# Kernel optimization log

Hardware: AMD Instinct MI355X
Metric: run time of the kernel (lower is better)

Reference implementation:

```python
import jax, jax.numpy as jnp
import numpy as np

HIDDEN = 2048
N_HEADS = 16
HEAD_DIM = HIDDEN // N_HEADS  # 128
ROTARY_DIM = 32
ROPE_BASE = 10000.0
NEG_INF = -10000.0  # matches torch code's additive mask constant


def setup_inputs() -> dict:
    key = jax.random.key(0)
    k1, k2, k3 = jax.random.split(key, 3)
    x = jax.random.normal(k1, (2, 2048, HIDDEN), dtype=jnp.float32)
    # scale weights like nn.Linear default init (uniform ~ 1/sqrt(fan_in))
    Wqkv_w = jax.random.normal(k2, (3 * HIDDEN, HIDDEN), dtype=jnp.float32) * (1.0 / np.sqrt(HIDDEN))
    Wqkv_b = jax.random.normal(k3, (3 * HIDDEN,), dtype=jnp.float32) * 0.01
    return {"x": x, "Wqkv_w": Wqkv_w, "Wqkv_b": Wqkv_b}


def _rope_cos_sin(seqlen, dtype):
    inv_freq = 1.0 / (ROPE_BASE ** (jnp.arange(0, ROTARY_DIM, 2, dtype=jnp.float32) / ROTARY_DIM))
    t = jnp.arange(seqlen, dtype=jnp.float32)
    freqs = jnp.outer(t, inv_freq)  # (S, ROTARY_DIM//2)
    return jnp.cos(freqs).astype(dtype), jnp.sin(freqs).astype(dtype)


def _apply_rotary(u, cos, sin):
    # u: (B, S, H, D); rotate first ROTARY_DIM dims, GPT-NeoX half-split style
    u_rot, u_pass = u[..., :ROTARY_DIM], u[..., ROTARY_DIM:]
    u1, u2 = u_rot[..., : ROTARY_DIM // 2], u_rot[..., ROTARY_DIM // 2 :]
    c = cos[None, :, None, :]  # (1, S, 1, ROTARY_DIM//2)
    s = sin[None, :, None, :]
    rot = jnp.concatenate([u1 * c - u2 * s, u1 * s + u2 * c], axis=-1)
    return jnp.concatenate([rot, u_pass], axis=-1)


def reference(x, Wqkv_w, Wqkv_b):
    B, S, _ = x.shape
    qkv = jnp.einsum("bse,oe->bso", x, Wqkv_w) + Wqkv_b  # (B, S, 3*H*D)
    qkv = qkv.reshape(B, S, 3, N_HEADS, HEAD_DIM)
    cos, sin = _rope_cos_sin(S, x.dtype)
    q = _apply_rotary(qkv[:, :, 0], cos, sin)
    k = _apply_rotary(qkv[:, :, 1], cos, sin)
    v = qkv[:, :, 2]
    scale = 1.0 / np.sqrt(HEAD_DIM)
    scores = jnp.einsum("bthd,bshd->bhts", q, k * scale)  # (B, H, T, S)
    causal_mask = jnp.triu(jnp.full((S, S), NEG_INF, dtype=scores.dtype), 1)
    scores = scores + causal_mask
    attn = jax.nn.softmax(scores, axis=-1)
    out = jnp.einsum("bhts,bshd->bthd", attn, v)  # (B, S, H, D)
    return out.reshape(B, S, N_HEADS * HEAD_DIM)
```

## Files before the change

### kernel.cpp

```cpp
#include <hip/hip_runtime.h>

#define B_    2
#define S_    2048
#define E_    2048
#define NH_   16
#define HD_   128
#define NQKV_ 6144
#define M_    4096
#define XN_   (M_ * E_)

typedef short bf16x8 __attribute__((ext_vector_type(8)));
typedef float f32x4  __attribute__((ext_vector_type(4)));

typedef const __attribute__((address_space(1))) void* gas_t;
typedef __attribute__((address_space(3))) void*       las_t;

__device__ inline float b2f(unsigned short u) {
    return __uint_as_float(((unsigned int)u) << 16);
}
__device__ inline unsigned short f2b(float f) {
    unsigned int x = __float_as_uint(f);
    x = x + 0x7fffu + ((x >> 16) & 1u);
    return (unsigned short)(x >> 16);
}
__device__ inline unsigned int pk2(float lo, float hi) {
    return (unsigned int)f2b(lo) | ((unsigned int)f2b(hi) << 16);
}

__global__ __launch_bounds__(256) void cvt_bf16(
    const float* __restrict__ X,
    const float* __restrict__ W,
    unsigned short* __restrict__ O)
{
    const long i = (long)(blockIdx.x * 256 + threadIdx.x) * 8;
    const float* src = (i < XN_) ? (X + i) : (W + (i - XN_));
    const float4 a = *(const float4*)(src);
    const float4 b = *(const float4*)(src + 4);
    uint4 o = { pk2(a.x, a.y), pk2(a.z, a.w), pk2(b.x, b.y), pk2(b.z, b.w) };
    *(uint4*)(O + i) = o;
}

__global__ __launch_bounds__(256, 2) void qkv_gemm(
    const unsigned short* __restrict__ Xb,
    const unsigned short* __restrict__ Wb,
    const float* __restrict__ bias,
    unsigned short* __restrict__ qb,
    unsigned short* __restrict__ kb,
    unsigned short* __restrict__ vb)
{
    __shared__ __align__(16) unsigned short As[2][128 * 32];
    __shared__ __align__(16) unsigned short Bs[2][128 * 32];

    const int t    = threadIdx.x;
    const int lane = t & 63;
    const int w    = t >> 6;
    const int m0   = blockIdx.y * 128;
    const int n0   = blockIdx.x * 128;
    const int wm   = (w >> 1) * 64;
    const int wn   = (w & 1) * 64;
    const int quad = lane >> 4;
    const int l16  = lane & 15;

    const unsigned short* Ag = Xb + (size_t)(m0 + (lane >> 2)) * E_ + (lane & 3) * 8;
    const unsigned short* Bg = Wb + (size_t)(n0 + (lane >> 2)) * E_ + (lane & 3) * 8;

    auto stage = [&](int bsel, int k0) {
        #pragma unroll
        for (int u = 0; u < 2; u++) {
            const int r0 = (w * 2 + u) * 16;
            __builtin_amdgcn_global_load_lds(
                (gas_t)(Ag + (size_t)r0 * E_ + k0),
                (las_t)&As[bsel][r0 * 32], 16, 0, 0);
            __builtin_amdgcn_global_load_lds(
                (gas_t)(Bg + (size_t)r0 * E_ + k0),
                (las_t)&Bs[bsel][r0 * 32], 16, 0, 0);
        }
    };

    f32x4 acc[4][4];
    #pragma unroll
    for (int i = 0; i < 4; i++)
        #pragma unroll
        for (int j = 0; j < 4; j++)
            #pragma unroll
            for (int r = 0; r < 4; r++) acc[i][j][r] = 0.0f;

    stage(0, 0);
    __syncthreads();
    int cur = 0;

    for (int k0 = 0; k0 < E_; k0 += 32) {
        if (k0 + 32 < E_) stage(cur ^ 1, k0 + 32);

        bf16x8 af[4], bfr[4];
        #pragma unroll
        for (int i = 0; i < 4; i++)
            af[i]  = *(const bf16x8*)&As[cur][(wm + i * 16 + l16) * 32 + quad * 8];
        #pragma unroll
        for (int i = 0; i < 4; i++)
            bfr[i] = *(const bf16x8*)&Bs[cur][(wn + i * 16 + l16) * 32 + quad * 8];

        #pragma unroll
        for (int i = 0; i < 4; i++)
            #pragma unroll
            for (int j = 0; j < 4; j++)
                acc[i][j] = __builtin_amdgcn_mfma_f32_16x16x32_bf16(
                    af[i], bfr[j], acc[i][j], 0, 0, 0);

        __syncthreads();
        cur ^= 1;
    }

    const int nb0   = n0 + wn;
    const int which = nb0 >> 11;
    const int h     = (nb0 >> 7) & 15;
    unsigned short* dst = (which == 0) ? qb : ((which == 1) ? kb : vb);

    float bv[4];
    #pragma unroll
    for (int j = 0; j < 4; j++) bv[j] = bias[nb0 + j * 16 + l16];
    #pragma unroll
    for (int i = 0; i < 4; i++)
        #pragma unroll
        for (int j = 0; j < 4; j++)
            #pragma unroll
            for (int r = 0; r < 4; r++) acc[i][j][r] += bv[j];

    if (wn == 0 && which < 2) {
        const float inv = exp2f(-0.83048202372184059f * (float)l16);
        #pragma unroll
        for (int i = 0; i < 4; i++) {
            #pragma unroll
            for (int r = 0; r < 4; r++) {
                const int m = m0 + wm + i * 16 + quad * 4 + r;
                const int s = m & (S_ - 1);
                float c, sn;
                __sincosf((float)s * inv, &sn, &c);
                const float u1 = acc[i][0][r], u2 = acc[i][1][r];
                acc[i][0][r] = u1 * c - u2 * sn;
                acc[i][1][r] = u1 * sn + u2 * c;
            }
        }
    }

    #pragma unroll
    for (int j = 0; j < 4; j++) {
        const int d = wn + j * 16 + l16;
        #pragma unroll
        for (int i = 0; i < 4; i++) {
            #pragma unroll
            for (int r = 0; r < 4; r++) {
                const int m  = m0 + wm + i * 16 + quad * 4 + r;
                const int bb = m >> 11;
                const int s  = m & (S_ - 1);
                dst[((size_t)(bb * NH_ + h) * S_ + s) * HD_ + d] = f2b(acc[i][j][r]);
            }
        }
    }
}

#define KSTR 136
#define VSTR 72
#define PSTR 72
#define OSTR 132

__global__ __launch_bounds__(256, 2) void attn_mfma(
    const unsigned short* __restrict__ qb,
    const unsigned short* __restrict__ kb,
    const unsigned short* __restrict__ vb,
    float* __restrict__ out)
{
    union SM {
        struct {
            unsigned short Ks[64 * KSTR];
            unsigned short Vt[128 * VSTR];
            unsigned short Ps[4 * 32 * PSTR];
        } a;
        float Ow[4 * 16 * OSTR];
    };
    __shared__ __align__(16) SM sm;
    unsigned short* Ks = sm.a.Ks;
    unsigned short* Vt = sm.a.Vt;
    unsigned short* Ps = sm.a.Ps;

    const int bid  = blockIdx.x;
    const int qt   = (S_ / 128 - 1) - (bid >> 5);
    const int bh   = bid & 31;
    const int b    = bh >> 4;
    const int h    = bh & 15;
    const int t    = threadIdx.x;
    const int lane = t & 63;
    const int w    = t >> 6;
    const int quad = lane >> 4;
    const int l16  = lane & 15;

    const int qb0    = qt * 128;
    const int wrow0  = qb0 + w * 32;
    const int ntiles = 2 * qt + 2;

    unsigned short* Pw = Ps + w * 32 * PSTR;

    const int krow = t >> 2, kcb = (t & 3) * 32;
    const int vq   = t & 31, vd0 = (t >> 5) * 16;

    bf16x8 qf[2][4];
    #pragma unroll
    for (int mb = 0; mb < 2; mb++) {
        const unsigned short* qp =
            qb + ((size_t)(bh * S_ + wrow0 + mb * 16 + l16)) * HD_ + quad * 8;
        #pragma unroll
        for (int c = 0; c < 4; c++)
            qf[mb][c] = *(const bf16x8*)(qp + c * 32);
    }

    f32x4 of[2][8];
    #pragma unroll
    for (int mb = 0; mb < 2; mb++)
        #pragma unroll
        for (int db = 0; db < 8; db++)
            #pragma unroll
            for (int r = 0; r < 4; r++) of[mb][db][r] = 0.0f;
    float mr[2][4], lr[2][4];
    #pragma unroll
    for (int mb = 0; mb < 2; mb++)
        #pragma unroll
        for (int r = 0; r < 4; r++) { mr[mb][r] = -1e30f; lr[mb][r] = 0.0f; }

    const float scale2 = 0.12751744459892879f;
    const float mneg2  = -14426.950408889634f;

    uint4 kr[4];
    uint4 v0a, v0b, v1a, v1b;

    auto issue_tile = [&](int kt2) {
        const int s2 = kt2 * 64;
        const unsigned short* kg = kb + ((size_t)(bh * S_ + s2 + krow)) * HD_ + kcb;
        #pragma unroll
        for (int u = 0; u < 4; u++) kr[u] = *(const uint4*)(kg + u * 8);
        const unsigned short* vg = vb + ((size_t)(bh * S_ + s2 + 2 * vq)) * HD_ + vd0;
        v0a = *(const uint4*)(vg);
        v0b = *(const uint4*)(vg + 8);
        v1a = *(const uint4*)(vg + HD_);
        v1b = *(const uint4*)(vg + HD_ + 8);
    };

    issue_tile(0);

    for (int kt = 0; kt < ntiles; kt++) {
        const int s0 = kt * 64;
        __syncthreads();
        #pragma unroll
        for (int u = 0; u < 4; u++)
            *(uint4*)&Ks[krow * KSTR + kcb + u * 8] = kr[u];
        {
            unsigned int r0[8] = { v0a.x, v0a.y, v0a.z, v0a.w,
                                   v0b.x, v0b.y, v0b.z, v0b.w };
            unsigned int r1[8] = { v1a.x, v1a.y, v1a.z, v1a.w,
                                   v1b.x, v1b.y, v1b.z, v1b.w };
            #pragma unroll
            for (int j = 0; j < 16; j++) {
                const int u = j >> 1;
                unsigned int pk;
                if ((j & 1) == 0)
                    pk = (r0[u] & 0xffffu) | (r1[u] << 16);
                else
                    pk = (r0[u] >> 16) | (r1[u] & 0xffff0000u);
                *(unsigned int*)&Vt[(vd0 + j) * VSTR + 2 * vq] = pk;
            }
        }
        __syncthreads();

        if (kt + 1 < ntiles) issue_tile(kt + 1);

        f32x4 sf[2][4];
        #pragma unroll
        for (int mb = 0; mb < 2; mb++)
            #pragma unroll
            for (int nb = 0; nb < 4; nb++)
                #pragma unroll
                for (int r = 0; r < 4; r++) sf[mb][nb][r] = 0.0f;
        #pragma unroll
        for (int c = 0; c < 4; c++) {
            #pragma unroll
            for (int nb = 0; nb < 4; nb++) {
                bf16x8 kf = *(const bf16x8*)&Ks[(nb * 16 + l16) * KSTR + c * 32 + quad * 8];
                #pragma unroll
                for (int mb = 0; mb < 2; mb++)
                    sf[mb][nb] = __builtin_amdgcn_mfma_f32_16x16x32_bf16(
                        qf[mb][c], kf, sf[mb][nb], 0, 0, 0);
            }
        }

        const bool need_mask = (s0 + 63 > wrow0);
        #pragma unroll
        for (int mb = 0; mb < 2; mb++) {
            const int qr0 = wrow0 + mb * 16 + quad * 4;
            #pragma unroll
            for (int nb = 0; nb < 4; nb++) {
                const int kcol = s0 + nb * 16 + l16;
                #pragma unroll
                for (int r = 0; r < 4; r++) {
                    float s = sf[mb][nb][r] * scale2;
                    if (need_mask && kcol > qr0 + r) s += mneg2;
                    sf[mb][nb][r] = s;
                }
            }
        }

        #pragma unroll
        for (int mb = 0; mb < 2; mb++) {
            float mt4[4];
            #pragma unroll
            for (int r = 0; r < 4; r++) {
                float mt = fmaxf(fmaxf(sf[mb][0][r], sf[mb][1][r]),
                                 fmaxf(sf[mb][2][r], sf[mb][3][r]));
                mt = fmaxf(mt, __shfl_xor(mt, 1));
                mt = fmaxf(mt, __shfl_xor(mt, 2));
                mt = fmaxf(mt, __shfl_xor(mt, 4));
                mt = fmaxf(mt, __shfl_xor(mt, 8));
                mt4[r] = mt;
            }
            const bool grew = (mt4[0] > mr[mb][0]) || (mt4[1] > mr[mb][1]) ||
                              (mt4[2] > mr[mb][2]) || (mt4[3] > mr[mb][3]);
            if (__any(grew)) {
                float alpha[4];
                #pragma unroll
                for (int r = 0; r < 4; r++) {
                    const float mnew = fmaxf(mr[mb][r], mt4[r]);
                    alpha[r] = __builtin_amdgcn_exp2f(mr[mb][r] - mnew);
                    mr[mb][r] = mnew;
                    lr[mb][r] *= alpha[r];
                }
                #pragma unroll
                for (int db = 0; db < 8; db++)
                    #pragma unroll
                    for (int r = 0; r < 4; r++) of[mb][db][r] *= alpha[r];
            }
            #pragma unroll
            for (int r = 0; r < 4; r++) {
                float rs = 0.0f;
                #pragma unroll
                for (int nb = 0; nb < 4; nb++) {
                    float p = __builtin_amdgcn_exp2f(sf[mb][nb][r] - mr[mb][r]);
                    sf[mb][nb][r] = p;
                    rs += p;
                }
                lr[mb][r] += rs;
            }

            #pragma unroll
            for (int nb = 0; nb < 4; nb++)
                #pragma unroll
                for (int r = 0; r < 4; r++)
                    Pw[(mb * 16 + quad * 4 + r) * PSTR + nb * 16 + l16] =
                        f2b(sf[mb][nb][r]);
        }

        #pragma unroll
        for (int kc = 0; kc < 2; kc++) {
            bf16x8 pf[2];
            #pragma unroll
            for (int mb = 0; mb < 2; mb++)
                pf[mb] = *(const bf16x8*)&Pw[(mb * 16 + l16) * PSTR + kc * 32 + quad * 8];
            #pragma unroll
            for (int db = 0; db < 8; db++) {
                bf16x8 vf = *(const bf16x8*)&Vt[(db * 16 + l16) * VSTR + kc * 32 + quad * 8];
                #pragma unroll
                for (int mb = 0; mb < 2; mb++)
                    of[mb][db] = __builtin_amdgcn_mfma_f32_16x16x32_bf16(
                        pf[mb], vf, of[mb][db], 0, 0, 0);
            }
        }
    }

    float* Ow = sm.Ow + w * 16 * OSTR;
    #pragma unroll
    for (int mb = 0; mb < 2; mb++) {
        __syncthreads();
        float inv[4];
        #pragma unroll
        for (int r = 0; r < 4; r++) {
            float ls = lr[mb][r];
            ls += __shfl_xor(ls, 1);
            ls += __shfl_xor(ls, 2);
            ls += __shfl_xor(ls, 4);
            ls += __shfl_xor(ls, 8);
            inv[r] = 1.0f / ls;
        }
        #pragma unroll
        for (int db = 0; db < 8; db++)
            #pragma unroll
            for (int r = 0; r < 4; r++)
                Ow[(quad * 4 + r) * OSTR + db * 16 + l16] = of[mb][db][r] * inv[r];
        #pragma unroll
        for (int rg = 0; rg < 4; rg++) {
            const int rowl = rg * 4 + quad;
            float* op = out + ((size_t)(b * S_ + wrow0 + mb * 16 + rowl)) * E_ + h * HD_;
            #pragma unroll
            for (int u = 0; u < 2; u++) {
                float4 v4 = *(const float4*)&Ow[rowl * OSTR + u * 64 + l16 * 4];
                *(float4*)(op + u * 64 + l16 * 4) = v4;
            }
        }
    }
}

extern "C" void kernel_launch(void* const* d_in, const int* in_sizes, int n_in,
                              void* d_out, int out_size, void* d_ws, size_t ws_size,
                              hipStream_t stream)
{
    const float* x    = (const float*)d_in[0];
    const float* W    = (const float*)d_in[1];
    const float* bias = (const float*)d_in[2];
    float* out = (float*)d_out;

    const size_t per = (size_t)B_ * NH_ * S_ * HD_;
    unsigned short* qb = (unsigned short*)d_ws;
    unsigned short* kb = qb + per;
    unsigned short* vb = kb + per;
    unsigned short* Xb = vb + per;
    unsigned short* Wb = Xb + (size_t)XN_;

    const int cvt_elems = XN_ + NQKV_ * E_;
    cvt_bf16<<<cvt_elems / (256 * 8), 256, 0, stream>>>(x, W, Xb);

    dim3 gemm_grid(NQKV_ / 128, M_ / 128);
    qkv_gemm<<<gemm_grid, 256, 0, stream>>>(Xb, Wb, bias, qb, kb, vb);

    attn_mfma<<<dim3((S_ / 128) * B_ * NH_), 256, 0, stream>>>(qb, kb, vb, out);
}
```

Measured before the change: 381.6 us.

## Shrink attention query tile to 64 rows per block, doubling grid size

Each attention block now handles 64 query rows (16 per wave) instead of 128 (32 per wave), and the grid grows to 1024 blocks. Per-thread accumulators and the P staging buffer are halved, and launch bounds now request 3 blocks per CU, aiming for better occupancy and load balance on the causal triangle. In exchange, every K/V tile is loaded and transposed into LDS once per 64 query rows rather than per 128, which doubles K/V global and LDS traffic, and each loaded K fragment now feeds only one MFMA instead of two.

After: 366.0 us. 4.1% less time.

```diff
diff --git a/kernel.cpp b/kernel.cpp
--- a/kernel.cpp
+++ b/kernel.cpp
@@ -164,7 +164,7 @@
 #define PSTR 72
 #define OSTR 132
 
-__global__ __launch_bounds__(256, 2) void attn_mfma(
+__global__ __launch_bounds__(256, 3) void attn_mfma(
     const unsigned short* __restrict__ qb,
     const unsigned short* __restrict__ kb,
     const unsigned short* __restrict__ vb,
@@ -174,7 +174,7 @@
         struct {
             unsigned short Ks[64 * KSTR];
             unsigned short Vt[128 * VSTR];
-            unsigned short Ps[4 * 32 * PSTR];
+            unsigned short Ps[4 * 16 * PSTR];
         } a;
         float Ow[4 * 16 * OSTR];
     };
@@ -184,7 +184,7 @@
     unsigned short* Ps = sm.a.Ps;
 
     const int bid  = blockIdx.x;
-    const int qt   = (S_ / 128 - 1) - (bid >> 5);
+    const int qt   = 31 - (bid >> 5);
     const int bh   = bid & 31;
     const int b    = bh >> 4;
     const int h    = bh & 15;
@@ -194,37 +194,31 @@
     const int quad = lane >> 4;
     const int l16  = lane & 15;
 
-    const int qb0    = qt * 128;
-    const int wrow0  = qb0 + w * 32;
-    const int ntiles = 2 * qt + 2;
-
-    unsigned short* Pw = Ps + w * 32 * PSTR;
+    const int wrow0  = qt * 64 + w * 16;
+    const int ntiles = qt + 1;
+
+    unsigned short* Pw = Ps + w * 16 * PSTR;
 
     const int krow = t >> 2, kcb = (t & 3) * 32;
     const int vq   = t & 31, vd0 = (t >> 5) * 16;
 
-    bf16x8 qf[2][4];
-    #pragma unroll
-    for (int mb = 0; mb < 2; mb++) {
+    bf16x8 qf[4];
+    {
         const unsigned short* qp =
-            qb + ((size_t)(bh * S_ + wrow0 + mb * 16 + l16)) * HD_ + quad * 8;
+            qb + ((size_t)(bh * S_ + wrow0 + l16)) * HD_ + quad * 8;
         #pragma unroll
         for (int c = 0; c < 4; c++)
-            qf[mb][c] = *(const bf16x8*)(qp + c * 32);
-    }
-
-    f32x4 of[2][8];
-    #pragma unroll
-    for (int mb = 0; mb < 2; mb++)
-        #pragma unroll
-        for (int db = 0; db < 8; db++)
-            #pragma unroll
-            for (int r = 0; r < 4; r++) of[mb][db][r] = 0.0f;
-    float mr[2][4], lr[2][4];
-    #pragma unroll
-    for (int mb = 0; mb < 2; mb++)
-        #pragma unroll
-        for (int r = 0; r < 4; r++) { mr[mb][r] = -1e30f; lr[mb][r] = 0.0f; }
+            qf[c] = *(const bf16x8*)(qp + c * 32);
+    }
+
+    f32x4 of[8];
+    #pragma unroll
+    for (int db = 0; db < 8; db++)
+        #pragma unroll
+        for (int r = 0; r < 4; r++) of[db][r] = 0.0f;
+    float mr[4], lr[4];
+    #pragma unroll
+    for (int r = 0; r < 4; r++) { mr[r] = -1e30f; lr[r] = 0.0f; }
 
     const float scale2 = 0.12751744459892879f;
     const float mneg2  = -14426.950408889634f;
@@ -272,135 +266,120 @@
 
         if (kt + 1 < ntiles) issue_tile(kt + 1);
 
-        f32x4 sf[2][4];
-        #pragma unroll
-        for (int mb = 0; mb < 2; mb++)
-            #pragma unroll
-            for (int nb = 0; nb < 4; nb++)
-                #pragma unroll
-                for (int r = 0; r < 4; r++) sf[mb][nb][r] = 0.0f;
+        f32x4 sf[4];
+        #pragma unroll
+        for (int nb = 0; nb < 4; nb++)
+            #pragma unroll
+            for (int r = 0; r < 4; r++) sf[nb][r] = 0.0f;
         #pragma unroll
         for (int c = 0; c < 4; c++) {
             #pragma unroll
             for (int nb = 0; nb < 4; nb++) {
                 bf16x8 kf = *(const bf16x8*)&Ks[(nb * 16 + l16) * KSTR + c * 32 + quad * 8];
-                #pragma unroll
-                for (int mb = 0; mb < 2; mb++)
-                    sf[mb][nb] = __builtin_amdgcn_mfma_f32_16x16x32_bf16(
-                        qf[mb][c], kf, sf[mb][nb], 0, 0, 0);
+                sf[nb] = __builtin_amdgcn_mfma_f32_16x16x32_bf16(
+                    qf[c], kf, sf[nb], 0, 0, 0);
             }
         }
 
         const bool need_mask = (s0 + 63 > wrow0);
-        #pragma unroll
-        for (int mb = 0; mb < 2; mb++) {
-            const int qr0 = wrow0 + mb * 16 + quad * 4;
+        {
+            const int qr0 = wrow0 + quad * 4;
             #pragma unroll
             for (int nb = 0; nb < 4; nb++) {
                 const int kcol = s0 + nb * 16 + l16;
                 #pragma unroll
                 for (int r = 0; r < 4; r++) {
-                    float s = sf[mb][nb][r] * scale2;
+                    float s = sf[nb][r] * scale2;
                     if (need_mask && kcol > qr0 + r) s += mneg2;
-                    sf[mb][nb][r] = s;
+                    sf[nb][r] = s;
                 }
             }
         }
 
-        #pragma unroll
-        for (int mb = 0; mb < 2; mb++) {
+        {
             float mt4[4];
             #pragma unroll
             for (int r = 0; r < 4; r++) {
-                float mt = fmaxf(fmaxf(sf[mb][0][r], sf[mb][1][r]),
-                                 fmaxf(sf[mb][2][r], sf[mb][3][r]));
+                float mt = fmaxf(fmaxf(sf[0][r], sf[1][r]),
+                                 fmaxf(sf[2][r], sf[3][r]));
                 mt = fmaxf(mt, __shfl_xor(mt, 1));
                 mt = fmaxf(mt, __shfl_xor(mt, 2));
                 mt = fmaxf(mt, __shfl_xor(mt, 4));
                 mt = fmaxf(mt, __shfl_xor(mt, 8));
                 mt4[r] = mt;
             }
-            const bool grew = (mt4[0] > mr[mb][0]) || (mt4[1] > mr[mb][1]) ||
-                              (mt4[2] > mr[mb][2]) || (mt4[3] > mr[mb][3]);
+            const bool grew = (mt4[0] > mr[0]) || (mt4[1] > mr[1]) ||
+                              (mt4[2] > mr[2]) || (mt4[3] > mr[3]);
             if (__any(grew)) {
                 float alpha[4];
                 #pragma unroll
                 for (int r = 0; r < 4; r++) {
-                    const float mnew = fmaxf(mr[mb][r], mt4[r]);
-                    alpha[r] = __builtin_amdgcn_exp2f(mr[mb][r] - mnew);
-                    mr[mb][r] = mnew;
-                    lr[mb][r] *= alpha[r];
+                    const float mnew = fmaxf(mr[r], mt4[r]);
+                    alpha[r] = __builtin_amdgcn_exp2f(mr[r] - mnew);
+                    mr[r] = mnew;
+                    lr[r] *= alpha[r];
                 }
                 #pragma unroll
                 for (int db = 0; db < 8; db++)
                     #pragma unroll
-                    for (int r = 0; r < 4; r++) of[mb][db][r] *= alpha[r];
+                    for (int r = 0; r < 4; r++) of[db][r] *= alpha[r];
             }
             #pragma unroll
             for (int r = 0; r < 4; r++) {
                 float rs = 0.0f;
                 #pragma unroll
                 for (int nb = 0; nb < 4; nb++) {
-                    float p = __builtin_amdgcn_exp2f(sf[mb][nb][r] - mr[mb][r]);
-                    sf[mb][nb][r] = p;
+                    float p = __builtin_amdgcn_exp2f(sf[nb][r] - mr[r]);
+                    sf[nb][r] = p;
                     rs += p;
                 }
-                lr[mb][r] += rs;
+                lr[r] += rs;
             }
 
             #pragma unroll
             for (int nb = 0; nb < 4; nb++)
                 #pragma unroll
                 for (int r = 0; r < 4; r++)
-                    Pw[(mb * 16 + quad * 4 + r) * PSTR + nb * 16 + l16] =
-                        f2b(sf[mb][nb][r]);
+                    Pw[(quad * 4 + r) * PSTR + nb * 16 + l16] = f2b(sf[nb][r]);
         }
 
         #pragma unroll
         for (int kc = 0; kc < 2; kc++) {
-            bf16x8 pf[2];
-            #pragma unroll
-            for (int mb = 0; mb < 2; mb++)
-                pf[mb] = *(const bf16x8*)&Pw[(mb * 16 + l16) * PSTR + kc * 32 + quad * 8];
+            bf16x8 pf = *(const bf16x8*)&Pw[l16 * PSTR + kc * 32 + quad * 8];
             #pragma unroll
             for (int db = 0; db < 8; db++) {
                 bf16x8 vf = *(const bf16x8*)&Vt[(db * 16 + l16) * VSTR + kc * 32 + quad * 8];
-                #pragma unroll
-                for (int mb = 0; mb < 2; mb++)
-                    of[mb][db] = __builtin_amdgcn_mfma_f32_16x16x32_bf16(
-                        pf[mb], vf, of[mb][db], 0, 0, 0);
+                of[db] = __builtin_amdgcn_mfma_f32_16x16x32_bf16(
+                    pf, vf, of[db], 0, 0, 0);
             }
         }
     }
 
     float* Ow = sm.Ow + w * 16 * OSTR;
-    #pragma unroll
-    for (int mb = 0; mb < 2; mb++) {
-        __syncthreads();
-        float inv[4];
-        #pragma unroll
-        for (int r = 0; r < 4; r++) {
-            float ls = lr[mb][r];
-            ls += __shfl_xor(ls, 1);
-            ls += __shfl_xor(ls, 2);
-            ls += __shfl_xor(ls, 4);
-            ls += __shfl_xor(ls, 8);
-            inv[r] = 1.0f / ls;
-        }
-        #pragma unroll
-        for (int db = 0; db < 8; db++)
-            #pragma unroll
-            for (int r = 0; r < 4; r++)
-                Ow[(quad * 4 + r) * OSTR + db * 16 + l16] = of[mb][db][r] * inv[r];
-        #pragma unroll
-        for (int rg = 0; rg < 4; rg++) {
-            const int rowl = rg * 4 + quad;
-            float* op = out + ((size_t)(b * S_ + wrow0 + mb * 16 + rowl)) * E_ + h * HD_;
-            #pragma unroll
-            for (int u = 0; u < 2; u++) {
-                float4 v4 = *(const float4*)&Ow[rowl * OSTR + u * 64 + l16 * 4];
-                *(float4*)(op + u * 64 + l16 * 4) = v4;
-            }
+    __syncthreads();
+    float inv[4];
+    #pragma unroll
+    for (int r = 0; r < 4; r++) {
+        float ls = lr[r];
+        ls += __shfl_xor(ls, 1);
+        ls += __shfl_xor(ls, 2);
+        ls += __shfl_xor(ls, 4);
+        ls += __shfl_xor(ls, 8);
+        inv[r] = 1.0f / ls;
+    }
+    #pragma unroll
+    for (int db = 0; db < 8; db++)
+        #pragma unroll
+        for (int r = 0; r < 4; r++)
+            Ow[(quad * 4 + r) * OSTR + db * 16 + l16] = of[db][r] * inv[r];
+    #pragma unroll
+    for (int rg = 0; rg < 4; rg++) {
+        const int rowl = rg * 4 + quad;
+        float* op = out + ((size_t)(b * S_ + wrow0 + rowl)) * E_ + h * HD_;
+        #pragma unroll
+        for (int u = 0; u < 2; u++) {
+            float4 v4 = *(const float4*)&Ow[rowl * OSTR + u * 64 + l16 * 4];
+            *(float4*)(op + u * 64 + l16 * 4) = v4;
         }
     }
 }
@@ -427,5 +406,5 @@
     dim3 gemm_grid(NQKV_ / 128, M_ / 128);
     qkv_gemm<<<gemm_grid, 256, 0, stream>>>(Xb, Wb, bias, qb, kb, vb);
 
-    attn_mfma<<<dim3((S_ / 128) * B_ * NH_), 256, 0, stream>>>(qb, kb, vb, out);
-}
+    attn_mfma<<<dim3(32 * 32), 256, 0, stream>>>(qb, kb, vb, out);
+}
```
